# Performance work log

Measured on AMD Instinct MI355X. Metric: run time of the kernel, lower is better.

The kernel has to match this reference:

```python
import jax, jax.numpy as jnp
import numpy as np

K = 20

def knn_idx(x, k):
    # x: [N, D] -> indices of k nearest neighbors (excluding self), [N, k]
    sq = jnp.sum(x * x, axis=-1)
    d = sq[:, None] + sq[None, :] - 2.0 * (x @ x.T)
    n = x.shape[0]
    d = d.at[jnp.arange(n), jnp.arange(n)].set(jnp.inf)
    _, idx = jax.lax.top_k(-d, k)
    return idx

def edge_conv(x, W, b, k):
    # DynamicEdgeConv: feat = [x_i, x_j - x_i] -> MLP -> max over neighbors
    idx = knn_idx(x, k)                      # [N, k]
    xj = x[idx]                              # [N, k, D]
    xi = jnp.broadcast_to(x[:, None, :], xj.shape)
    feat = jnp.concatenate([xi, xj - xi], axis=-1)   # [N, k, 2D]
    h = jax.nn.relu(feat @ W + b)            # [N, k, C]
    return jnp.max(h, axis=1)                # [N, C]

def dilate_flat(x, W, b, k):
    # DilateFlatEdgeConv: flat morphological dilation (max over kNN) + MLP
    idx = knn_idx(x, k)
    dil = jnp.max(x[idx], axis=1)            # [N, C]
    return jax.nn.relu(dil @ W + b)

def setup_inputs() -> dict:
    key = jax.random.key(0)
    ks = jax.random.split(key, 12)
    N, C, NC = 8192, 64, 16
    s = 0.05
    return {
        "x": jax.random.normal(ks[0], (N, 3), dtype=jnp.float32),
        "W1": jax.random.normal(ks[1], (6, C), dtype=jnp.float32) * s,
        "b1": jnp.zeros((C,), jnp.float32),
        "Wd1": jax.random.normal(ks[2], (C, C), dtype=jnp.float32) * s,
        "bd1": jnp.zeros((C,), jnp.float32),
        "Wd2": jax.random.normal(ks[3], (C, C), dtype=jnp.float32) * s,
        "bd2": jnp.zeros((C,), jnp.float32),
        "Wd3": jax.random.normal(ks[4], (C, C), dtype=jnp.float32) * s,
        "bd3": jnp.zeros((C,), jnp.float32),
        "Wl": jax.random.normal(ks[5], (3 * C, 1024), dtype=jnp.float32) * s,
        "bl": jnp.zeros((1024,), jnp.float32),
        "Wm1": jax.random.normal(ks[6], (1024, 256), dtype=jnp.float32) * s,
        "bm1": jnp.zeros((256,), jnp.float32),
        "Wm2": jax.random.normal(ks[7], (256, 128), dtype=jnp.float32) * s,
        "bm2": jnp.zeros((128,), jnp.float32),
        "Wm3": jax.random.normal(ks[8], (128, NC), dtype=jnp.float32) * s,
        "bm3": jnp.zeros((NC,), jnp.float32),
    }

def reference(x, W1, b1, Wd1, bd1, Wd2, bd2, Wd3, bd3, Wl, bl, Wm1, bm1, Wm2, bm2, Wm3, bm3):
    x_feat = edge_conv(x, W1, b1, K)          # [N, 64]
    x1 = dilate_flat(x_feat, Wd1, bd1, K) - x_feat
    x2 = dilate_flat(x1, Wd2, bd2, K) - x1
    x3 = dilate_flat(x2, Wd3, bd3, K) - x2
    h = jax.nn.relu(jnp.concatenate([x1, x2, x3], axis=1) @ Wl + bl)  # [N, 1024]
    h = jax.nn.relu(h @ Wm1 + bm1)            # dropout is identity at eval
    h = jax.nn.relu(h @ Wm2 + bm2)
    logits = h @ Wm3 + bm3
    return jax.nn.log_softmax(logits, axis=-1)
```

## Files before the change

### kernel.cpp

```cpp
#include <hip/hip_runtime.h>
#include <math.h>

#define NPTS 8192
#define KNN 20
#define KSEL 8
#define CAPD3 256
#define CAP64 512
#define LCAP 2048
#define LCAPM 1024

typedef __attribute__((ext_vector_type(8))) short bf16x8;
typedef __attribute__((ext_vector_type(16))) float f32x16;

__device__ __forceinline__ uint32_t fkey(float v) {
  uint32_t b = __float_as_uint(v);
  return b ^ ((uint32_t)((int)b >> 31) | 0x80000000u);
}
__device__ __forceinline__ float unkey(uint32_t k) {
  uint32_t b = (k & 0x80000000u) ? (k ^ 0x80000000u) : ~k;
  return __uint_as_float(b);
}
__device__ __forceinline__ ushort f2bf(float v) {
  uint32_t u = __float_as_uint(v);
  u += 0x7FFFu + ((u >> 16) & 1u);
  return (ushort)(u >> 16);
}
__device__ __forceinline__ float bf2f(ushort h) {
  return __uint_as_float(((uint32_t)h) << 16);
}

__device__ __forceinline__ void insert8k(uint32_t (&d)[KSEL], uint32_t key) {
#pragma unroll
  for (int r = 0; r < KSEL; ++r) {
    uint32_t nd = min(d[r], key);
    key = max(d[r], key);
    d[r] = nd;
  }
}

__global__ void sqnorm_kernel(const float* __restrict__ x, int ldx, int D,
                              float* __restrict__ sq,
                              unsigned int* __restrict__ nmax2u) {
  int i = blockIdx.x * blockDim.x + threadIdx.x;
  if (i >= NPTS) return;
  const float* xr = x + (size_t)i * ldx;
  float s = 0.f;
  for (int d = 0; d < D; ++d) { float v = xr[d]; s += v * v; }
  sq[i] = s;
  atomicMax(nmax2u, __float_as_uint(s));
}

__global__ __launch_bounds__(256) void tobf16_kernel(
    const float* __restrict__ x, int ldx, ushort* __restrict__ xh,
    ushort* __restrict__ xl) {
  const int i = blockIdx.x * 256 + threadIdx.x;
  const int row = (i * 8) >> 6, col = (i * 8) & 63;
  const float* src = &x[(size_t)row * ldx + col];
  ushort oh[8], ol[8];
#pragma unroll
  for (int e = 0; e < 8; ++e) {
    float v = src[e];
    ushort h = f2bf(v);
    oh[e] = h;
    ol[e] = f2bf(v - bf2f(h));
  }
  *(ushort4*)&xh[(size_t)row * 64 + col] =
      make_ushort4(oh[0], oh[1], oh[2], oh[3]);
  *(ushort4*)&xh[(size_t)row * 64 + col + 4] =
      make_ushort4(oh[4], oh[5], oh[6], oh[7]);
  *(ushort4*)&xl[(size_t)row * 64 + col] =
      make_ushort4(ol[0], ol[1], ol[2], ol[3]);
  *(ushort4*)&xl[(size_t)row * 64 + col + 4] =
      make_ushort4(ol[4], ol[5], ol[6], ol[7]);
}

#define WRITE_S(QR, BASE)                                                   \
  {                                                                         \
    const int cc = (4 * bg) & 31;                                           \
    const int jbase = cb + (QR)*32 + cc;                                    \
    _Pragma("unroll") for (int u = 0; u < 8; ++u) {                         \
      const int row = 4 * am + (u & 3) + 64 * (u >> 2);                     \
      const int gq = qb * 128 + row;                                        \
      const int sw = ((row & 7) ^ ((row >> 2) & 7)) << 2;                   \
      uint32_t k0 = fkey(fmaf(-2.f, acc[u][(BASE) + 0], sc[(BASE) + 0]));   \
      uint32_t k1 = fkey(fmaf(-2.f, acc[u][(BASE) + 1], sc[(BASE) + 1]));   \
      uint32_t k2 = fkey(fmaf(-2.f, acc[u][(BASE) + 2], sc[(BASE) + 2]));   \
      uint32_t k3 = fkey(fmaf(-2.f, acc[u][(BASE) + 3], sc[(BASE) + 3]));   \
      if (jbase + 0 == gq) k0 = 0xFFFFFFFFu;                                \
      if (jbase + 1 == gq) k1 = 0xFFFFFFFFu;                                \
      if (jbase + 2 == gq) k2 = 0xFFFFFFFFu;                                \
      if (jbase + 3 == gq) k3 = 0xFFFFFFFFu;                                \
      *(uint4*)&S[row * 32 + (cc ^ sw)] = make_uint4(k0, k1, k2, k3);       \
    }                                                                       \
  }

#define COMMIT_CS()                                                         \
  {                                                                         \
    Cs[(ck + 0) * 128 + cn] = p0.x;  Cs[(ck + 1) * 128 + cn] = p0.y;        \
    Cs[(ck + 2) * 128 + cn] = p0.z;  Cs[(ck + 3) * 128 + cn] = p0.w;        \
    Cs[(ck + 4) * 128 + cn] = p1.x;  Cs[(ck + 5) * 128 + cn] = p1.y;        \
    Cs[(ck + 6) * 128 + cn] = p1.z;  Cs[(ck + 7) * 128 + cn] = p1.w;        \
    Cs[(ck + 8) * 128 + cn] = p2.x;  Cs[(ck + 9) * 128 + cn] = p2.y;        \
    Cs[(ck + 10) * 128 + cn] = p2.z; Cs[(ck + 11) * 128 + cn] = p2.w;       \
    Cs[(ck + 12) * 128 + cn] = p3.x; Cs[(ck + 13) * 128 + cn] = p3.y;       \
    Cs[(ck + 14) * 128 + cn] = p3.z; Cs[(ck + 15) * 128 + cn] = p3.w;       \
  }

#define ISSUE_CS(BASEROW, KOFF)                                             \
  {                                                                         \
    const float* src_ = &x[(size_t)((BASEROW) + cn) * LDX + (KOFF) + ck];   \
    p0 = *(const float4*)&src_[0];                                          \
    p1 = *(const float4*)&src_[4];                                          \
    p2 = *(const float4*)&src_[8];                                          \
    p3 = *(const float4*)&src_[12];                                         \
  }

template <int LDX>
__global__ __launch_bounds__(256, 2) void knn_gemm_kernel(
    const float* __restrict__ x, const float* __restrict__ sq,
    uint32_t* __restrict__ pk) {
  __shared__ float Qs[64 * 128];
  __shared__ uint32_t CsS[32 * 128];
  float* const Cs = (float*)CsS;
  uint32_t* const S = CsS;
  const int t = threadIdx.x;
  const int qb = blockIdx.x;
  const int ch = blockIdx.y;
  const int am = t & 15;
  const int bg = (t >> 4) & 15;
  const int cn = t & 127;
  const int ck = (t >> 7) * 16;

  {
    const int q = t & 127;
    const int k0 = (t >> 7) * 32;
    const float* src = &x[(size_t)(qb * 128 + q) * LDX + k0];
#pragma unroll
    for (int c = 0; c < 8; ++c) {
      float4 v = *(const float4*)&src[c * 4];
      Qs[(k0 + c * 4 + 0) * 128 + q] = v.x;
      Qs[(k0 + c * 4 + 1) * 128 + q] = v.y;
      Qs[(k0 + c * 4 + 2) * 128 + q] = v.z;
      Qs[(k0 + c * 4 + 3) * 128 + q] = v.w;
    }
  }

  const int selq = t & 127, part = t >> 7;
  uint32_t dreg[KSEL];
#pragma unroll
  for (int r = 0; r < KSEL; ++r) dreg[r] = 0xFFFFFFFFu;

  float4 p0, p1, p2, p3;
  ISSUE_CS(ch * 256, 0)

#pragma unroll 1
  for (int tile = 0; tile < 2; ++tile) {
    const int cb = ch * 256 + tile * 128;
    float acc[8][8] = {};
#pragma unroll
    for (int kh = 0; kh < 2; ++kh) {
      __syncthreads();
      COMMIT_CS()
      if (kh == 0) {
        ISSUE_CS(cb, 32)
      } else if (tile == 0) {
        ISSUE_CS(cb + 128, 0)
      }
      __syncthreads();
#pragma unroll 4
      for (int k2 = 0; k2 < 32; ++k2) {
        const int k = kh * 32 + k2;
        float4 A0 = *(const float4*)&Qs[k * 128 + 4 * am];
        float4 A1 = *(const float4*)&Qs[k * 128 + 4 * am + 64];
        float4 B0 = *(const float4*)&Cs[k2 * 128 + 4 * bg];
        float4 B1 = *(const float4*)&Cs[k2 * 128 + 4 * bg + 64];
        float a[8] = {A0.x, A0.y, A0.z, A0.w, A1.x, A1.y, A1.z, A1.w};
        float b[8] = {B0.x, B0.y, B0.z, B0.w, B1.x, B1.y, B1.z, B1.w};
#pragma unroll
        for (int u = 0; u < 8; ++u)
#pragma unroll
          for (int v = 0; v < 8; ++v) acc[u][v] = fmaf(a[u], b[v], acc[u][v]);
      }
    }
    float4 s0 = *(const float4*)&sq[cb + 4 * bg];
    float4 s1 = *(const float4*)&sq[cb + 4 * bg + 64];
    float sc[8] = {s0.x, s0.y, s0.z, s0.w, s1.x, s1.y, s1.z, s1.w};

    const int qlow = bg >> 3;
    for (int qr = 0; qr < 4; ++qr) {
      __syncthreads();
      if (qr == qlow) WRITE_S(qr, 0);
      if (qr == 2 + qlow) WRITE_S(qr, 4);
      __syncthreads();
      const int swr = ((selq & 7) ^ ((selq >> 2) & 7)) << 2;
#pragma unroll
      for (int g_ = 0; g_ < 4; ++g_) {
        const int cc = part * 16 + g_ * 4;
        uint4 sv = *(const uint4*)&S[selq * 32 + (cc ^ swr)];
        uint32_t kv[4] = {sv.x, sv.y, sv.z, sv.w};
#pragma unroll
        for (int e = 0; e < 4; ++e) {
          if (kv[e] < dreg[KSEL - 1]) insert8k(dreg, kv[e]);
        }
      }
    }
  }
  const int l = ch * 2 + part;
  uint32_t* pkq = pk + ((size_t)l * NPTS + (qb * 128 + selq)) * KSEL;
#pragma unroll
  for (int r = 0; r < KSEL; ++r) pkq[r] = dreg[r];
}

__global__ __launch_bounds__(256) void knn_mergeT_kernel(
    const uint32_t* __restrict__ pk, const float* __restrict__ sq,
    const float* __restrict__ nmax2, float* __restrict__ Tf, float mscale) {
  __shared__ uint32_t sk[16][16][KSEL];
  const int t = threadIdx.x;
  const int ql = t >> 4;
  const int l = t & 15;
  const int q = blockIdx.x * 16 + ql;
  const uint32_t* pkq = pk + ((size_t)l * NPTS + q) * KSEL;
#pragma unroll
  for (int r = 0; r < KSEL; ++r) sk[ql][l][r] = pkq[r];
  __syncthreads();
  int ptr = 0;
  uint32_t k = 0;
#pragma unroll 1
  for (int s = 0; s < KNN; ++s) {
    k = (ptr < KSEL) ? sk[ql][l][ptr] : 0xFFFFFFFFu;
    int src = l;
#pragma unroll
    for (int off = 8; off >= 1; off >>= 1) {
      uint32_t ok = __shfl_xor(k, off, 16);
      int osrc = __shfl_xor(src, off, 16);
      bool take = (ok < k) || (ok == k && osrc < src);
      k = take ? ok : k;
      src = take ? osrc : src;
    }
    if (l == src) ptr++;
  }
  if (l == 0) Tf[q] = unkey(k) + mscale * sqrtf(sq[q] * nmax2[0]);
}

__global__ __launch_bounds__(256, 2) void knn_recover_mfma_kernel(
    const ushort* __restrict__ xh, const ushort* __restrict__ xl,
    const float* __restrict__ sq, const float* __restrict__ Tf,
    uint32_t* __restrict__ cnt, int* __restrict__ cj) {
  __shared__ ushort Ah_s[128 * 72];
  __shared__ ushort Al_s[128 * 72];
  __shared__ ushort Bh_s[64 * 72];
  __shared__ ushort Bl_s[64 * 72];
  __shared__ uint32_t nsurv;
  __shared__ uint2 surv[LCAPM];
  const int t = threadIdx.x;
  const int w = t >> 6, l = t & 63;
  const int qbase = blockIdx.x * 128;
  const int cbase = blockIdx.y * 64;
  const int q0 = qbase + w * 32;
  const int lr = l & 31;
  const int ko = (l >> 5) * 8;
  const int rowbase = (l >> 5) * 4;

  if (t == 0) nsurv = 0;

  {
    const int row = t >> 1, half = t & 1;
    const uint4* sh = (const uint4*)&xh[(size_t)(qbase + row) * 64 + half * 32];
    const uint4* sl = (const uint4*)&xl[(size_t)(qbase + row) * 64 + half * 32];
    uint4* dh = (uint4*)&Ah_s[row * 72 + half * 32];
    uint4* dl = (uint4*)&Al_s[row * 72 + half * 32];
#pragma unroll
    for (int i = 0; i < 4; ++i) { dh[i] = sh[i]; dl[i] = sl[i]; }
  }
  {
    const int pl = t >> 7;
    const int rr = (t & 127) >> 1, half = t & 1;
    const ushort* src = pl ? xl : xh;
    ushort* dst = pl ? Bl_s : Bh_s;
    const uint4* s = (const uint4*)&src[(size_t)(cbase + rr) * 64 + half * 32];
    uint4* d = (uint4*)&dst[rr * 72 + half * 32];
#pragma unroll
    for (int i = 0; i < 4; ++i) d[i] = s[i];
  }

  float tq[16];
#pragma unroll
  for (int r = 0; r < 16; ++r)
    tq[r] = Tf[q0 + (r & 3) + 8 * (r >> 2) + rowbase];

  __syncthreads();

  f32x16 acc[2] = {};
#pragma unroll
  for (int kk = 0; kk < 4; ++kk) {
    const int cu = kk * 16 + ko;
    bf16x8 Ah, Al, Bh[2], Bl[2];
    {
      const int row = w * 32 + lr;
      Ah = *(const bf16x8*)&Ah_s[row * 72 + cu];
      Al = *(const bf16x8*)&Al_s[row * 72 + cu];
    }
#pragma unroll
    for (int ct = 0; ct < 2; ++ct) {
      const int row = ct * 32 + lr;
      Bh[ct] = *(const bf16x8*)&Bh_s[row * 72 + cu];
      Bl[ct] = *(const bf16x8*)&Bl_s[row * 72 + cu];
    }
#pragma unroll
    for (int ct = 0; ct < 2; ++ct) {
      acc[ct] = __builtin_amdgcn_mfma_f32_32x32x16_bf16(Ah, Bh[ct], acc[ct],
                                                        0, 0, 0);
      acc[ct] = __builtin_amdgcn_mfma_f32_32x32x16_bf16(Ah, Bl[ct], acc[ct],
                                                        0, 0, 0);
      acc[ct] = __builtin_amdgcn_mfma_f32_32x32x16_bf16(Al, Bh[ct], acc[ct],
                                                        0, 0, 0);
    }
  }

#pragma unroll
  for (int ct = 0; ct < 2; ++ct) {
    const int j = cbase + ct * 32 + lr;
    const float sqj = sq[j];
#pragma unroll
    for (int r = 0; r < 16; ++r) {
      const int gq = q0 + (r & 3) + 8 * (r >> 2) + rowbase;
      float d = fmaf(-2.f, acc[ct][r], sqj);
      if (j != gq && d <= tq[r]) {
        uint32_t idx = atomicAdd(&nsurv, 1u);
        if (idx < (uint32_t)LCAPM) {
          surv[idx] = make_uint2((uint32_t)gq, (uint32_t)j);
        } else {
          uint32_t slot = atomicAdd(&cnt[gq], 1u);
          if (slot < (uint32_t)CAP64) cj[(size_t)gq * CAP64 + slot] = j;
        }
      }
    }
  }
  __syncthreads();
  const uint32_t nv = min(nsurv, (uint32_t)LCAPM);
#pragma unroll 1
  for (uint32_t i = t; i < nv; i += 256) {
    uint2 e = surv[i];
    uint32_t slot = atomicAdd(&cnt[e.x], 1u);
    if (slot < (uint32_t)CAP64) cj[(size_t)e.x * CAP64 + slot] = (int)e.y;
  }
}

template <int LDX>
__global__ __launch_bounds__(256) void knn_final64_kernel(
    const float* __restrict__ x, const float* __restrict__ sq,
    const uint32_t* __restrict__ cnt, const int* __restrict__ cj,
    int* __restrict__ idx_out) {
  __shared__ float xqs[4][64];
  const int t = threadIdx.x, w = t >> 6, l = t & 63;
  const int q = blockIdx.x * 4 + w;
  if (l < 16)
    *(float4*)&xqs[w][l * 4] = *(const float4*)&x[(size_t)q * LDX + l * 4];
  __syncthreads();
  const int n = (int)min(cnt[q], (uint32_t)CAP64);
  uint32_t ks[8]; int js[8];
#pragma unroll
  for (int r = 0; r < 8; ++r) { ks[r] = 0xFFFFFFFFu; js[r] = 0x7fffffff; }
#pragma unroll 1
  for (int it = 0; it < 8; ++it) {
    const int c = l + it * 64;
    if (c < n) {
      const int j = cj[(size_t)q * CAP64 + c];
      const float* xj = &x[(size_t)j * LDX];
      float dot = 0.f;
#pragma unroll
      for (int e = 0; e < 16; ++e) {
        float4 a = *(const float4*)&xj[e * 4];
        float4 b = *(const float4*)&xqs[w][e * 4];
        dot = fmaf(a.x, b.x, dot);
        dot = fmaf(a.y, b.y, dot);
        dot = fmaf(a.z, b.z, dot);
        dot = fmaf(a.w, b.w, dot);
      }
      float d = fmaf(-2.f, dot, sq[j]);
      uint32_t ck = fkey(d);
      int ci = j;
#pragma unroll
      for (int r = 0; r < 8; ++r) {
        bool sw = (ck < ks[r]) || (ck == ks[r] && ci < js[r]);
        uint32_t ok = ks[r]; int oj = js[r];
        ks[r] = sw ? ck : ok; js[r] = sw ? ci : oj;
        ck = sw ? ok : ck; ci = sw ? oj : ci;
      }
    }
  }
#pragma unroll 1
  for (int s = 0; s < KNN; ++s) {
    uint32_t mk = ks[0];
    int mj = js[0];
#pragma unroll
    for (int off = 32; off >= 1; off >>= 1) {
      uint32_t ok = __shfl_xor(mk, off, 64);
      int oj = __shfl_xor(mj, off, 64);
      bool take = (ok < mk) || (ok == mk && oj < mj);
      mk = take ? ok : mk;
      mj = take ? oj : mj;
    }
    if (ks[0] == mk && js[0] == mj) {
#pragma unroll
      for (int r = 0; r < 7; ++r) { ks[r] = ks[r + 1]; js[r] = js[r + 1]; }
      ks[7] = 0xFFFFFFFFu; js[7] = 0x7fffffff;
    }
    if (l == 0) idx_out[(size_t)q * KNN + s] = mj;
  }
}

__global__ __launch_bounds__(256) void knn_d3k_kernel(
    const float* __restrict__ x, const float* __restrict__ sq,
    uint32_t* __restrict__ pk) {
  __shared__ float4 Ct[128];
  const int t = threadIdx.x;
  const int q = blockIdx.x * 256 + t;
  const int ch = blockIdx.y;
  const int cb = ch * 128;
  if (t < 128)
    Ct[t] = make_float4(x[(cb + t) * 3], x[(cb + t) * 3 + 1],
                        x[(cb + t) * 3 + 2], sq[cb + t]);
  const float xi0 = x[q * 3], xi1 = x[q * 3 + 1], xi2 = x[q * 3 + 2];
  uint32_t dreg[KSEL];
#pragma unroll
  for (int r = 0; r < KSEL; ++r) dreg[r] = 0xFFFFFFFFu;
  __syncthreads();
#pragma unroll 1
  for (int c = 0; c < 128; ++c) {
    float4 cv = Ct[c];
    int j = cb + c;
    float val = fmaf(-2.f, xi0 * cv.x + xi1 * cv.y + xi2 * cv.z, cv.w);
    uint32_t key = fkey(val);
    if (j != q && key < dreg[KSEL - 1]) insert8k(dreg, key);
  }
  uint32_t* pkq = pk + ((size_t)ch * NPTS + q) * KSEL;
#pragma unroll
  for (int r = 0; r < KSEL; ++r) pkq[r] = dreg[r];
}

__global__ __launch_bounds__(256) void knn_d3_recover_kernel(
    const float* __restrict__ x, const float* __restrict__ sq,
    const float* __restrict__ Tf, uint32_t* __restrict__ cnt,
    uint32_t* __restrict__ cd, int* __restrict__ cj) {
  __shared__ float4 Ct[256];
  __shared__ uint32_t nsurv;
  __shared__ uint2 surv[LCAP];
  const int t = threadIdx.x;
  const int q0 = blockIdx.x * 256;
  const int q = q0 + t;
  const int cb = blockIdx.y * 256;
  if (t == 0) nsurv = 0;
  Ct[t] = make_float4(x[(cb + t) * 3], x[(cb + t) * 3 + 1],
                      x[(cb + t) * 3 + 2], sq[cb + t]);
  const float xi0 = x[q * 3], xi1 = x[q * 3 + 1], xi2 = x[q * 3 + 2];
  const float Tq = Tf[q];
  __syncthreads();
#pragma unroll 1
  for (int c = 0; c < 256; ++c) {
    float4 cv = Ct[c];
    int j = cb + c;
    float val = fmaf(-2.f, xi0 * cv.x + xi1 * cv.y + xi2 * cv.z, cv.w);
    if (j != q && val <= Tq) {
      uint32_t idx = atomicAdd(&nsurv, 1u);
      if (idx < (uint32_t)LCAP) {
        surv[idx] = make_uint2(fkey(val), ((uint32_t)t << 16) | (uint32_t)j);
      } else {
        uint32_t slot = atomicAdd(&cnt[q], 1u);
        if (slot < (uint32_t)CAPD3) {
          cd[(size_t)q * CAPD3 + slot] = fkey(val);
          cj[(size_t)q * CAPD3 + slot] = j;
        }
      }
    }
  }
  __syncthreads();
  const uint32_t nv = min(nsurv, (uint32_t)LCAP);
#pragma unroll 1
  for (uint32_t i = t; i < nv; i += 256) {
    uint2 e = surv[i];
    const int qq = q0 + (int)(e.y >> 16);
    const int jj = (int)(e.y & 0xFFFFu);
    uint32_t slot = atomicAdd(&cnt[qq], 1u);
    if (slot < (uint32_t)CAPD3) {
      cd[(size_t)qq * CAPD3 + slot] = e.x;
      cj[(size_t)qq * CAPD3 + slot] = jj;
    }
  }
}

#define CSWAP(ka, ja, kb, jb)                                   \
  {                                                             \
    bool sw = (kb < ka) || (kb == ka && jb < ja);               \
    uint32_t tk = sw ? kb : ka; int tj = sw ? jb : ja;          \
    kb = sw ? ka : kb; jb = sw ? ja : jb;                       \
    ka = tk; ja = tj;                                           \
  }

__global__ __launch_bounds__(256) void knn_final_d3_kernel(
    const uint32_t* __restrict__ cnt, const uint32_t* __restrict__ cd,
    const int* __restrict__ cj, int* __restrict__ idx_out) {
  const int t = threadIdx.x;
  const int w = t >> 6;
  const int l = t & 63;
  const int q = blockIdx.x * 4 + w;
  const int n = (int)min(cnt[q], (uint32_t)CAPD3);
  uint32_t k0 = 0xFFFFFFFFu, k1 = 0xFFFFFFFFu, k2 = 0xFFFFFFFFu,
           k3 = 0xFFFFFFFFu;
  int j0 = 0x7fffffff, j1 = 0x7fffffff, j2 = 0x7fffffff, j3 = 0x7fffffff;
  if (l < n) { k0 = cd[(size_t)q * CAPD3 + l]; j0 = cj[(size_t)q * CAPD3 + l]; }
  if (l + 64 < n) { k1 = cd[(size_t)q * CAPD3 + l + 64]; j1 = cj[(size_t)q * CAPD3 + l + 64]; }
  if (l + 128 < n) { k2 = cd[(size_t)q * CAPD3 + l + 128]; j2 = cj[(size_t)q * CAPD3 + l + 128]; }
  if (l + 192 < n) { k3 = cd[(size_t)q * CAPD3 + l + 192]; j3 = cj[(size_t)q * CAPD3 + l + 192]; }
  CSWAP(k0, j0, k1, j1); CSWAP(k2, j2, k3, j3);
  CSWAP(k0, j0, k2, j2); CSWAP(k1, j1, k3, j3);
  CSWAP(k1, j1, k2, j2);
#pragma unroll 1
  for (int s = 0; s < KNN; ++s) {
    uint32_t mk = k0;
    int mj = j0;
#pragma unroll
    for (int off = 32; off >= 1; off >>= 1) {
      uint32_t ok = __shfl_xor(mk, off, 64);
      int oj = __shfl_xor(mj, off, 64);
      bool take = (ok < mk) || (ok == mk && oj < mj);
      mk = take ? ok : mk;
      mj = take ? oj : mj;
    }
    if (k0 == mk && j0 == mj) {
      k0 = k1; j0 = j1; k1 = k2; j1 = j2; k2 = k3; j2 = j3;
      k3 = 0xFFFFFFFFu; j3 = 0x7fffffff;
    }
    if (l == 0) idx_out[(size_t)q * KNN + s] = mj;
  }
}

__global__ __launch_bounds__(256) void edgeconv_kernel(
    const float* __restrict__ x, const int* __restrict__ idx,
    const float* __restrict__ W1, const float* __restrict__ b1,
    float* __restrict__ out) {
  const int i = blockIdx.x * 4 + (threadIdx.x >> 6);
  const int c = threadIdx.x & 63;
  float w0 = W1[c], w1 = W1[64 + c], w2 = W1[128 + c];
  float w3 = W1[192 + c], w4 = W1[256 + c], w5 = W1[320 + c];
  float xi0 = x[3 * i], xi1 = x[3 * i + 1], xi2 = x[3 * i + 2];
  float base = b1[c] + xi0 * w0 + xi1 * w1 + xi2 * w2;
  float m = -INFINITY;
#pragma unroll
  for (int k = 0; k < KNN; ++k) {
    int j = idx[i * KNN + k];
    float d0 = x[3 * j] - xi0, d1 = x[3 * j + 1] - xi1, d2 = x[3 * j + 2] - xi2;
    float h = base + d0 * w3 + d1 * w4 + d2 * w5;
    m = fmaxf(m, fmaxf(h, 0.f));
  }
  out[(size_t)i * 64 + c] = m;
}

__global__ __launch_bounds__(256) void dilate_kernel(
    const float* __restrict__ xin, int ldin, const int* __restrict__ idx,
    const float* __restrict__ W, const float* __restrict__ bias,
    float* __restrict__ out, int ldout) {
  const int g = threadIdx.x >> 6;
  const int i = blockIdx.x * 4 + g;
  const int c = threadIdx.x & 63;
  __shared__ float dil[4][64];
  float m = -INFINITY;
#pragma unroll
  for (int k = 0; k < KNN; ++k) {
    int j = idx[i * KNN + k];
    m = fmaxf(m, xin[(size_t)j * ldin + c]);
  }
  dil[g][c] = m;
  __syncthreads();
  float acc = bias[c];
#pragma unroll
  for (int d = 0; d < 64; ++d) acc = fmaf(dil[g][d], W[d * 64 + c], acc);
  out[(size_t)i * ldout + c] = fmaxf(acc, 0.f) - xin[(size_t)i * ldin + c];
}

template <int BN>
__global__ __launch_bounds__(256) void gemm128_kernel(
    const float* __restrict__ A, int K, int ldA, const float* __restrict__ W,
    int N, const float* __restrict__ bias, float* __restrict__ C, int ldC,
    int relu) {
  constexpr int VN = BN / 16;
  __shared__ float As[16 * 128];
  __shared__ float Bs[16 * BN];
  const int t = threadIdx.x;
  const int bn = blockIdx.x * BN;
  const int bm = blockIdx.y * 128;
  const int am = t & 15;
  const int bg = (t >> 4) & 15;
  const int m_ = t & 127;
  const int ka = (t >> 7) * 8;
  const int kb = t >> 4;
  const int nb = (t & 15) * (BN == 128 ? 8 : 4);
  float acc[8][VN] = {};
  float4 av0, av1, bv0, bv1;

  {
    const float* srcA = &A[(size_t)(bm + m_) * ldA + ka];
    av0 = *(const float4*)&srcA[0];
    av1 = *(const float4*)&srcA[4];
    const float* srcB = &W[(size_t)kb * N + bn + nb];
    bv0 = *(const float4*)&srcB[0];
    if constexpr (BN == 128) bv1 = *(const float4*)&srcB[4];
  }

  for (int k0 = 0; k0 < K; k0 += 16) {
    __syncthreads();
    As[(ka + 0) * 128 + m_] = av0.x;
    As[(ka + 1) * 128 + m_] = av0.y;
    As[(ka + 2) * 128 + m_] = av0.z;
    As[(ka + 3) * 128 + m_] = av0.w;
    As[(ka + 4) * 128 + m_] = av1.x;
    As[(ka + 5) * 128 + m_] = av1.y;
    As[(ka + 6) * 128 + m_] = av1.z;
    As[(ka + 7) * 128 + m_] = av1.w;
    *(float4*)&Bs[kb * BN + nb] = bv0;
    if constexpr (BN == 128) *(float4*)&Bs[kb * BN + nb + 4] = bv1;
    if (k0 + 16 < K) {
      const float* srcA = &A[(size_t)(bm + m_) * ldA + k0 + 16 + ka];
      av0 = *(const float4*)&srcA[0];
      av1 = *(const float4*)&srcA[4];
      const float* srcB = &W[(size_t)(k0 + 16 + kb) * N + bn + nb];
      bv0 = *(const float4*)&srcB[0];
      if constexpr (BN == 128) bv1 = *(const float4*)&srcB[4];
    }
    __syncthreads();
#pragma unroll
    for (int k = 0; k < 16; ++k) {
      float4 A0 = *(const float4*)&As[k * 128 + 4 * am];
      float4 A1 = *(const float4*)&As[k * 128 + 4 * am + 64];
      float a[8] = {A0.x, A0.y, A0.z, A0.w, A1.x, A1.y, A1.z, A1.w};
      float b[VN];
      float4 B0 = *(const float4*)&Bs[k * BN + 4 * bg];
      b[0] = B0.x; b[1] = B0.y; b[2] = B0.z; b[3] = B0.w;
      if constexpr (BN == 128) {
        float4 B1 = *(const float4*)&Bs[k * BN + 4 * bg + 64];
        b[4] = B1.x; b[5] = B1.y; b[6] = B1.z; b[7] = B1.w;
      }
#pragma unroll
      for (int u = 0; u < 8; ++u)
#pragma unroll
        for (int v = 0; v < VN; ++v) acc[u][v] = fmaf(a[u], b[v], acc[u][v]);
    }
  }
#pragma unroll
  for (int u = 0; u < 8; ++u) {
    const int m = bm + 4 * am + (u & 3) + 64 * (u >> 2);
#pragma unroll
    for (int vq = 0; vq < VN / 4; ++vq) {
      const int n = bn + 4 * bg + 64 * vq;
      float4 o;
      float* po = (float*)&o;
#pragma unroll
      for (int e = 0; e < 4; ++e) {
        float val = acc[u][vq * 4 + e] + bias[n + e];
        po[e] = relu ? fmaxf(val, 0.f) : val;
      }
      *(float4*)&C[(size_t)m * ldC + n] = o;
    }
  }
}

__global__ __launch_bounds__(256) void final_kernel(
    const float* __restrict__ h3, const float* __restrict__ Wm3,
    const float* __restrict__ bm3, float* __restrict__ out) {
  __shared__ float hs[16][132];
  const int tid = threadIdx.x;
  const int r = tid >> 4, c = tid & 15;
  const int row0 = blockIdx.x * 16;
#pragma unroll
  for (int l = tid; l < 2048; l += 256)
    hs[l >> 7][l & 127] = h3[(size_t)row0 * 128 + l];
  __syncthreads();
  float acc = bm3[c];
#pragma unroll
  for (int d = 0; d < 128; ++d) acc = fmaf(hs[r][d], Wm3[d * 16 + c], acc);
  float mx = acc;
#pragma unroll
  for (int o = 8; o >= 1; o >>= 1) mx = fmaxf(mx, __shfl_xor(mx, o, 16));
  float e = expf(acc - mx);
  float s = e;
#pragma unroll
  for (int o = 8; o >= 1; o >>= 1) s += __shfl_xor(s, o, 16);
  out[(size_t)(row0 + r) * 16 + c] = (acc - mx) - logf(s);
}

extern "C" void kernel_launch(void* const* d_in, const int* in_sizes, int n_in,
                              void* d_out, int out_size, void* d_ws,
                              size_t ws_size, hipStream_t stream) {
  const float* x = (const float*)d_in[0];
  const float* W1 = (const float*)d_in[1];
  const float* b1 = (const float*)d_in[2];
  const float* Wd1 = (const float*)d_in[3];
  const float* bd1 = (const float*)d_in[4];
  const float* Wd2 = (const float*)d_in[5];
  const float* bd2 = (const float*)d_in[6];
  const float* Wd3 = (const float*)d_in[7];
  const float* bd3 = (const float*)d_in[8];
  const float* Wl = (const float*)d_in[9];
  const float* bl = (const float*)d_in[10];
  const float* Wm1 = (const float*)d_in[11];
  const float* bm1 = (const float*)d_in[12];
  const float* Wm2 = (const float*)d_in[13];
  const float* bm2 = (const float*)d_in[14];
  const float* Wm3 = (const float*)d_in[15];
  const float* bm3 = (const float*)d_in[16];
  float* out = (float*)d_out;

  char* ws = (char*)d_ws;
  float* sq = (float*)(ws + 0);
  int* idxA = (int*)(ws + 32768);
  float* xfeat = (float*)(ws + 1343488);
  float* xcat = (float*)(ws + 3440640);
  float* h1 = (float*)(ws + 9732096);
  float* h2 = (float*)(ws + 43286528);
  float* h3 = (float*)(ws + 51675136);
  float* x1 = xcat;
  float* x2 = xcat + 64;
  float* x3 = xcat + 128;
  uint32_t* pk = (uint32_t*)(ws + 9732096);
  uint32_t* cdD3 = (uint32_t*)(ws + 13926400);
  int* cjD3 = (int*)(ws + 22315008);
  float* Tf = (float*)(ws + 30703616);
  uint32_t* cnt = (uint32_t*)(ws + 30736384);
  unsigned int* nmax2u = (unsigned int*)(ws + 30769152);
  float* nmax2f = (float*)nmax2u;
  int* cj64 = (int*)(ws + 30769216);
  ushort* xh = (ushort*)(ws + 47546432);
  ushort* xl = (ushort*)(ws + 48595008);

  hipMemsetAsync(cnt, 0, 32768 + 64, stream);
  sqnorm_kernel<<<32, 256, 0, stream>>>(x, 3, 3, sq, nmax2u);
  knn_d3k_kernel<<<dim3(32, 16), 256, 0, stream>>>(x, sq, pk);
  knn_mergeT_kernel<<<NPTS / 16, 256, 0, stream>>>(pk, sq, nmax2f, Tf, 0.f);
  knn_d3_recover_kernel<<<dim3(32, 32), 256, 0, stream>>>(x, sq, Tf, cnt,
                                                          cdD3, cjD3);
  knn_final_d3_kernel<<<NPTS / 4, 256, 0, stream>>>(cnt, cdD3, cjD3, idxA);
  edgeconv_kernel<<<NPTS / 4, 256, 0, stream>>>(x, idxA, W1, b1, xfeat);

#define KNN64_PASS(XIN, LDX)                                                  \
  hipMemsetAsync(cnt, 0, 32768 + 64, stream);                                 \
  sqnorm_kernel<<<32, 256, 0, stream>>>(XIN, LDX, 64, sq, nmax2u);            \
  tobf16_kernel<<<256, 256, 0, stream>>>(XIN, LDX, xh, xl);                   \
  knn_gemm_kernel<LDX><<<dim3(64, 8), 256, 0, stream>>>(XIN, sq, pk);         \
  knn_mergeT_kernel<<<NPTS / 16, 256, 0, stream>>>(pk, sq, nmax2f, Tf,        \
                                                   1e-4f);                    \
  knn_recover_mfma_kernel<<<dim3(64, 128), 256, 0, stream>>>(xh, xl, sq, Tf,  \
                                                             cnt, cj64);      \
  knn_final64_kernel<LDX><<<NPTS / 4, 256, 0, stream>>>(XIN, sq, cnt, cj64,   \
                                                        idxA);

  KNN64_PASS(xfeat, 64)
  dilate_kernel<<<NPTS / 4, 256, 0, stream>>>(xfeat, 64, idxA, Wd1, bd1, x1,
                                              192);
  KNN64_PASS(x1, 192)
  dilate_kernel<<<NPTS / 4, 256, 0, stream>>>(x1, 192, idxA, Wd2, bd2, x2,
                                              192);
  KNN64_PASS(x2, 192)
  dilate_kernel<<<NPTS / 4, 256, 0, stream>>>(x2, 192, idxA, Wd3, bd3, x3,
                                              192);
#undef KNN64_PASS

  gemm128_kernel<128><<<dim3(1024 / 128, NPTS / 128), 256, 0, stream>>>(
      xcat, 192, 192, Wl, 1024, bl, h1, 1024, 1);
  gemm128_kernel<64><<<dim3(256 / 64, NPTS / 128), 256, 0, stream>>>(
      h1, 1024, 1024, Wm1, 256, bm1, h2, 256, 1);
  gemm128_kernel<64><<<dim3(128 / 64, NPTS / 128), 256, 0, stream>>>(
      h2, 256, 256, Wm2, 128, bm2, h3, 128, 1);
  final_kernel<<<NPTS / 16, 256, 0, stream>>>(h3, Wm3, bm3, out);
}
```

Baseline: 917.1 us.

## Loop recover kernel over eight candidate tiles, reusing A tile and prefetching B

Each block of the MFMA recover kernel now walks 512 candidate columns in eight 64-wide steps instead of handling a single 64-column tile, so the query A tile is loaded into LDS once and reused. The next B tile is prefetched into registers while the current one is computed. The grid shrinks from 64x128 to 64x16 blocks, which cuts per-block setup and redundant A loads. In exchange there is less parallelism, extra barriers per iteration, and the shared survivor buffer is now shared across all eight tiles, so it overflows to global atomics more often.

```diff
diff --git a/kernel.cpp b/kernel.cpp
--- a/kernel.cpp
+++ b/kernel.cpp
@@ -7,7 +7,7 @@
 #define CAPD3 256
 #define CAP64 512
 #define LCAP 2048
-#define LCAPM 1024
+#define LCAPR 1024
 
 typedef __attribute__((ext_vector_type(8))) short bf16x8;
 typedef __attribute__((ext_vector_type(16))) float f32x16;
@@ -251,15 +251,19 @@
   __shared__ ushort Bh_s[64 * 72];
   __shared__ ushort Bl_s[64 * 72];
   __shared__ uint32_t nsurv;
-  __shared__ uint2 surv[LCAPM];
+  __shared__ uint2 surv[LCAPR];
   const int t = threadIdx.x;
   const int w = t >> 6, l = t & 63;
   const int qbase = blockIdx.x * 128;
-  const int cbase = blockIdx.y * 64;
+  const int cgrp = blockIdx.y * 512;
   const int q0 = qbase + w * 32;
   const int lr = l & 31;
   const int ko = (l >> 5) * 8;
   const int rowbase = (l >> 5) * 4;
+
+  const int bpl = t >> 7;
+  const int brr = (t & 127) >> 1;
+  const int bhalf = t & 1;
 
   if (t == 0) nsurv = 0;
 
@@ -272,72 +276,89 @@
 #pragma unroll
     for (int i = 0; i < 4; ++i) { dh[i] = sh[i]; dl[i] = sl[i]; }
   }
-  {
-    const int pl = t >> 7;
-    const int rr = (t & 127) >> 1, half = t & 1;
-    const ushort* src = pl ? xl : xh;
-    ushort* dst = pl ? Bl_s : Bh_s;
-    const uint4* s = (const uint4*)&src[(size_t)(cbase + rr) * 64 + half * 32];
-    uint4* d = (uint4*)&dst[rr * 72 + half * 32];
-#pragma unroll
-    for (int i = 0; i < 4; ++i) d[i] = s[i];
-  }
 
   float tq[16];
 #pragma unroll
   for (int r = 0; r < 16; ++r)
     tq[r] = Tf[q0 + (r & 3) + 8 * (r >> 2) + rowbase];
 
+  uint4 pb[4];
+  {
+    const ushort* src = bpl ? xl : xh;
+    const uint4* s = (const uint4*)&src[(size_t)(cgrp + brr) * 64 + bhalf * 32];
+#pragma unroll
+    for (int i = 0; i < 4; ++i) pb[i] = s[i];
+  }
   __syncthreads();
 
-  f32x16 acc[2] = {};
-#pragma unroll
-  for (int kk = 0; kk < 4; ++kk) {
-    const int cu = kk * 16 + ko;
-    bf16x8 Ah, Al, Bh[2], Bl[2];
+#pragma unroll 1
+  for (int it = 0; it < 8; ++it) {
+    const int cbase = cgrp + it * 64;
     {
-      const int row = w * 32 + lr;
-      Ah = *(const bf16x8*)&Ah_s[row * 72 + cu];
-      Al = *(const bf16x8*)&Al_s[row * 72 + cu];
-    }
+      ushort* dst = bpl ? Bl_s : Bh_s;
+      uint4* d = (uint4*)&dst[brr * 72 + bhalf * 32];
+#pragma unroll
+      for (int i = 0; i < 4; ++i) d[i] = pb[i];
+    }
+    if (it < 7) {
+      const ushort* src = bpl ? xl : xh;
+      const uint4* s =
+          (const uint4*)&src[(size_t)(cbase + 64 + brr) * 64 + bhalf * 32];
+#pragma unroll
+      for (int i = 0; i < 4; ++i) pb[i] = s[i];
+    }
+    __syncthreads();
+
+    f32x16 acc[2] = {};
+#pragma unroll
+    for (int kk = 0; kk < 4; ++kk) {
+      const int cu = kk * 16 + ko;
+      bf16x8 Ah, Al, Bh[2], Bl[2];
+      {
+        const int row = w * 32 + lr;
+        Ah = *(const bf16x8*)&Ah_s[row * 72 + cu];
+        Al = *(const bf16x8*)&Al_s[row * 72 + cu];
+      }
+#pragma unroll
+      for (int ct = 0; ct < 2; ++ct) {
+        const int row = ct * 32 + lr;
+        Bh[ct] = *(const bf16x8*)&Bh_s[row * 72 + cu];
+        Bl[ct] = *(const bf16x8*)&Bl_s[row * 72 + cu];
+      }
+#pragma unroll
+      for (int ct = 0; ct < 2; ++ct) {
+        acc[ct] = __builtin_amdgcn_mfma_f32_32x32x16_bf16(Ah, Bh[ct], acc[ct],
+                                                          0, 0, 0);
+        acc[ct] = __builtin_amdgcn_mfma_f32_32x32x16_bf16(Ah, Bl[ct], acc[ct],
+                                                          0, 0, 0);
+        acc[ct] = __builtin_amdgcn_mfma_f32_32x32x16_bf16(Al, Bh[ct], acc[ct],
+                                                          0, 0, 0);
+      }
+    }
+
 #pragma unroll
     for (int ct = 0; ct < 2; ++ct) {
-      const int row = ct * 32 + lr;
-      Bh[ct] = *(const bf16x8*)&Bh_s[row * 72 + cu];
-      Bl[ct] = *(const bf16x8*)&Bl_s[row * 72 + cu];
-    }
-#pragma unroll
-    for (int ct = 0; ct < 2; ++ct) {
-      acc[ct] = __builtin_amdgcn_mfma_f32_32x32x16_bf16(Ah, Bh[ct], acc[ct],
-                                                        0, 0, 0);
-      acc[ct] = __builtin_amdgcn_mfma_f32_32x32x16_bf16(Ah, Bl[ct], acc[ct],
-                                                        0, 0, 0);
-      acc[ct] = __builtin_amdgcn_mfma_f32_32x32x16_bf16(Al, Bh[ct], acc[ct],
-                                                        0, 0, 0);
-    }
-  }
-
-#pragma unroll
-  for (int ct = 0; ct < 2; ++ct) {
-    const int j = cbase + ct * 32 + lr;
-    const float sqj = sq[j];
-#pragma unroll
-    for (int r = 0; r < 16; ++r) {
-      const int gq = q0 + (r & 3) + 8 * (r >> 2) + rowbase;
-      float d = fmaf(-2.f, acc[ct][r], sqj);
-      if (j != gq && d <= tq[r]) {
-        uint32_t idx = atomicAdd(&nsurv, 1u);
-        if (idx < (uint32_t)LCAPM) {
-          surv[idx] = make_uint2((uint32_t)gq, (uint32_t)j);
-        } else {
-          uint32_t slot = atomicAdd(&cnt[gq], 1u);
-          if (slot < (uint32_t)CAP64) cj[(size_t)gq * CAP64 + slot] = j;
+      const int j = cbase + ct * 32 + lr;
+      const float sqj = sq[j];
+#pragma unroll
+      for (int r = 0; r < 16; ++r) {
+        const int gq = q0 + (r & 3) + 8 * (r >> 2) + rowbase;
+        float d = fmaf(-2.f, acc[ct][r], sqj);
+        if (j != gq && d <= tq[r]) {
+          uint32_t idx = atomicAdd(&nsurv, 1u);
+          if (idx < (uint32_t)LCAPR) {
+            surv[idx] = make_uint2((uint32_t)gq, (uint32_t)j);
+          } else {
+            uint32_t slot = atomicAdd(&cnt[gq], 1u);
+            if (slot < (uint32_t)CAP64) cj[(size_t)gq * CAP64 + slot] = j;
+          }
         }
       }
     }
-  }
-  __syncthreads();
-  const uint32_t nv = min(nsurv, (uint32_t)LCAPM);
+    __syncthreads();
+  }
+
+  const uint32_t nv = min(nsurv, (uint32_t)LCAPR);
 #pragma unroll 1
   for (uint32_t i = t; i < nv; i += 256) {
     uint2 e = surv[i];
@@ -748,8 +769,8 @@
   knn_gemm_kernel<LDX><<<dim3(64, 8), 256, 0, stream>>>(XIN, sq, pk);         \
   knn_mergeT_kernel<<<NPTS / 16, 256, 0, stream>>>(pk, sq, nmax2f, Tf,        \
                                                    1e-4f);                    \
-  knn_recover_mfma_kernel<<<dim3(64, 128), 256, 0, stream>>>(xh, xl, sq, Tf,  \
-                                                             cnt, cj64);      \
+  knn_recover_mfma_kernel<<<dim3(64, 16), 256, 0, stream>>>(xh, xl, sq, Tf,   \
+                                                            cnt, cj64);       \
   knn_final64_kernel<LDX><<<NPTS / 4, 256, 0, stream>>>(XIN, sq, cnt, cj64,   \
                                                         idxA);
 
```

Result: no change. 915.5 us (-0.2%).
